# Optimization experiments

Hardware: AMD Instinct MI355X
Metric: run time of the kernel (lower is better)

Reference implementation:

```python
import jax, jax.numpy as jnp
import numpy as np

NEG_SLOPE = 0.2  # PyG GATConv default leaky_relu slope


def gat_layer(x, src, dst, W, a_src, a_dst, n_nodes, heads, ch):
    # x: [N, in_dim]; W: [in_dim, heads*ch]
    h = (x @ W).reshape(n_nodes, heads, ch)              # [N, H, C]
    e_s = jnp.einsum('nhc,hc->nh', h, a_src)             # [N, H]
    e_d = jnp.einsum('nhc,hc->nh', h, a_dst)             # [N, H]
    e = jax.nn.leaky_relu(e_s[src] + e_d[dst], NEG_SLOPE)  # [E, H]
    # segment softmax over incoming edges of each destination node
    m = jax.lax.stop_gradient(jax.ops.segment_max(e, dst, num_segments=n_nodes))
    w = jnp.exp(e - m[dst])                              # [E, H]
    z = jax.ops.segment_sum(w, dst, num_segments=n_nodes)  # [N, H]
    alpha = w / z[dst]                                   # [E, H]
    msg = h[src] * alpha[:, :, None]                     # [E, H, C]
    out = jax.ops.segment_sum(msg, dst, num_segments=n_nodes)  # [N, H, C]
    return out


def setup_inputs() -> dict:
    key = jax.random.key(0)
    ks = jax.random.split(key, 12)
    N, E, D, H = 50000, 800000, 128, 4
    x = jax.random.normal(ks[0], (N, D), dtype=jnp.float32)
    edge_index = jax.random.randint(ks[1], (2, E), 0, N, dtype=jnp.int64)
    s1 = 1.0 / np.sqrt(D)
    s2 = 1.0 / np.sqrt(D * H)
    W1 = jax.random.normal(ks[2], (D, H * D), dtype=jnp.float32) * s1
    a1_src = jax.random.normal(ks[3], (H, D), dtype=jnp.float32) * s1
    a1_dst = jax.random.normal(ks[4], (H, D), dtype=jnp.float32) * s1
    b1 = jax.random.normal(ks[5], (H * D,), dtype=jnp.float32) * 0.01
    W2 = jax.random.normal(ks[6], (H * D, D), dtype=jnp.float32) * s2
    a2_src = jax.random.normal(ks[7], (1, D), dtype=jnp.float32) * s1
    a2_dst = jax.random.normal(ks[8], (1, D), dtype=jnp.float32) * s1
    b2 = jax.random.normal(ks[9], (D,), dtype=jnp.float32) * 0.01
    fc_w = jax.random.normal(ks[10], (D, 1), dtype=jnp.float32) * s1
    fc_b = jax.random.normal(ks[11], (1,), dtype=jnp.float32) * 0.01
    return {"x": x, "edge_index": edge_index, "W1": W1, "a1_src": a1_src,
            "a1_dst": a1_dst, "b1": b1, "W2": W2, "a2_src": a2_src,
            "a2_dst": a2_dst, "b2": b2, "fc_w": fc_w, "fc_b": fc_b}


def reference(x, edge_index, W1, a1_src, a1_dst, b1, W2, a2_src, a2_dst, b2, fc_w, fc_b):
    N, D = x.shape
    H = a1_src.shape[0]
    # add self-loops (PyG GATConv default add_self_loops=True)
    loop = jnp.arange(N, dtype=edge_index.dtype)
    src = jnp.concatenate([edge_index[0], loop])
    dst = jnp.concatenate([edge_index[1], loop])
    # conv1: heads=4, concat=True -> [N, H*D]
    h1 = gat_layer(x, src, dst, W1, a1_src, a1_dst, N, H, D)
    h1 = jax.nn.relu(h1.reshape(N, H * D) + b1)
    # dropout p=0.2 is identity in eval mode
    # conv2: heads=1 -> [N, D]
    h2 = gat_layer(h1, src, dst, W2, a2_src, a2_dst, N, 1, D)
    h2 = h2.reshape(N, D) + b2
    return h2 @ fc_w + fc_b  # [N, 1]
```

## Files before the change

kernel.cpp:

```cpp
#include <hip/hip_runtime.h>
#include <cstdint>
#include <cstddef>

constexpr int kN   = 50000;
constexpr int kE   = 800000;
constexpr int kEt  = kE + kN;
constexpr float kSlope = 0.2f;
constexpr int kScanB = (kN + 255) / 256;
constexpr int kConvB = (kN * 16 + 255) / 256;
constexpr int kHistB = (kEt + 255) / 256;
constexpr int kQuarB = (kN * 16 + 255) / 256;

typedef __attribute__((ext_vector_type(8))) short bf8_t;
typedef __attribute__((ext_vector_type(4))) float f4_t;
typedef __attribute__((ext_vector_type(2))) float f2_t;

__device__ __align__(16) unsigned short g_xb[(size_t)kN * 128];
__device__ __align__(16) unsigned short g_aggx[(size_t)kN * 512];
__device__ __align__(16) unsigned short g_w1t[4 * 128 * 128];
__device__ __align__(16) float g_u[3][512];
__device__ __align__(16) float g_es1[kN * 4];
__device__ __align__(16) float g_ed1[kN * 4];
__device__ __align__(16) float2 g_sp[kN];
__device__ float g_ed2[kN];
__device__ float g_c0;
__device__ __align__(16) float g_p1s[4 * 128];
__device__ __align__(16) float g_p1d[4 * 128];
__device__ int g_deg[kN];
__device__ int g_ptr[kN + 1];
__device__ int g_rank[kEt];
__device__ int g_srcs[kEt];
__device__ int g_bsum[kScanB];

__device__ __forceinline__ float lrelu(float x) { return x > 0.f ? x : kSlope * x; }

__device__ __forceinline__ bf8_t bf8_zero() {
  uint4 z = make_uint4(0u, 0u, 0u, 0u);
  return *(bf8_t*)&z;
}

__device__ __forceinline__ unsigned short f2bf1(float v) {
  unsigned u = __float_as_uint(v);
  unsigned r = (u + 0x7FFFu + ((u >> 16) & 1u)) >> 16;
  return (unsigned short)r;
}

__global__ __launch_bounds__(256) void k_init(const float* __restrict__ x,
    const int* __restrict__ ei,
    const float* __restrict__ W1, const float* __restrict__ W2,
    const float* __restrict__ a1s, const float* __restrict__ a1d,
    const float* __restrict__ a2s, const float* __restrict__ a2d,
    const float* __restrict__ b2, const float* __restrict__ fcw,
    const float* __restrict__ fcb) {
  const int b = blockIdx.x, t = threadIdx.x;
  if (b < 197) {
    int i = b * 256 + t;
    if (i < kN) {
      g_sp[i] = make_float2(0.f, 0.f);
      g_ed2[i] = 0.f;
    }
  } else if (b < 453) {
    int gid = (b - 197) * 256 + t;
    int h = gid >> 14, rem = gid & 16383;
    int c = rem >> 7, j = rem & 127;
    float v = W1[(size_t)c * 512 + h * 128 + j];
    g_w1t[((size_t)h * 128 + j) * 128 + c] = f2bf1(v);
  } else if (b < 457) {
    int gid = (b - 453) * 256 + t;
    int which = gid >> 9, idx = gid & 511;
    int h = idx >> 7, k = idx & 127;
    const float* a = which ? a1d : a1s;
    const float* wrow = W1 + (size_t)k * 512 + h * 128;
    float s = 0.f;
#pragma unroll 8
    for (int c = 0; c < 128; ++c) s += wrow[c] * a[h * 128 + c];
    (which ? g_p1d : g_p1s)[idx] = s;
  } else if (b < 463) {
    int gid = (b - 457) * 256 + t;
    if (gid < 1536) {
      int v = gid >> 9, k = gid & 511;
      const float* vv = v == 0 ? a2s : v == 1 ? a2d : fcw;
      const float* wrow = W2 + (size_t)k * 128;
      float s = 0.f;
#pragma unroll 8
      for (int c = 0; c < 128; ++c) s += wrow[c] * vv[c];
      g_u[v][k] = s;
    }
  } else if (b < 464) {
    if (t < 64) {
      float s = b2[t] * fcw[t] + b2[64 + t] * fcw[64 + t];
#pragma unroll
      for (int off = 32; off > 0; off >>= 1) s += __shfl_down(s, off);
      if (t == 0) g_c0 = s + fcb[0];
    }
  } else if (b < 464 + kConvB) {
    int g = (b - 464) * 256 + t;
    if (g < kN * 16) {
      const float* xp = x + (size_t)g * 8;
      float4 f0 = *(const float4*)xp;
      float4 f1 = *(const float4*)(xp + 4);
      unsigned w0 = (unsigned)f2bf1(f0.x) | ((unsigned)f2bf1(f0.y) << 16);
      unsigned w1 = (unsigned)f2bf1(f0.z) | ((unsigned)f2bf1(f0.w) << 16);
      unsigned w2 = (unsigned)f2bf1(f1.x) | ((unsigned)f2bf1(f1.y) << 16);
      unsigned w3 = (unsigned)f2bf1(f1.z) | ((unsigned)f2bf1(f1.w) << 16);
      *(uint4*)(g_xb + (size_t)g * 8) = make_uint4(w0, w1, w2, w3);
    }
  } else {
    int e = (b - 464 - kConvB) * 256 + t;
    if (e < kEt) {
      int d = (e < kE) ? ei[kE + e] : e - kE;
      g_rank[e] = atomicAdd(&g_deg[d], 1);
    }
  }
}

__device__ __forceinline__ void scores1_body(const float* __restrict__ x,
                                             int bid, int t) {
  const int lane = t & 63;
  const int qt = lane >> 4, ql = lane & 15;
  const int n = ((bid * 256 + t) >> 6) * 4 + qt;
  if (n >= kN) return;
  const float* xp = x + (size_t)n * 128 + ql * 8;
  float4 xa = *(const float4*)xp;
  float4 xb = *(const float4*)(xp + 4);
  float s[4], d[4];
#pragma unroll
  for (int h = 0; h < 4; ++h) {
    const float* ps = g_p1s + h * 128 + ql * 8;
    const float* pd = g_p1d + h * 128 + ql * 8;
    s[h] = xa.x * ps[0] + xa.y * ps[1] + xa.z * ps[2] + xa.w * ps[3]
         + xb.x * ps[4] + xb.y * ps[5] + xb.z * ps[6] + xb.w * ps[7];
    d[h] = xa.x * pd[0] + xa.y * pd[1] + xa.z * pd[2] + xa.w * pd[3]
         + xb.x * pd[4] + xb.y * pd[5] + xb.z * pd[6] + xb.w * pd[7];
  }
#pragma unroll
  for (int off = 1; off < 16; off <<= 1) {
#pragma unroll
    for (int h = 0; h < 4; ++h) {
      s[h] += __shfl_xor(s[h], off);
      d[h] += __shfl_xor(d[h], off);
    }
  }
  if (ql == 0) {
    *(float4*)(g_es1 + (size_t)n * 4) = make_float4(s[0], s[1], s[2], s[3]);
    *(float4*)(g_ed1 + (size_t)n * 4) = make_float4(d[0], d[1], d[2], d[3]);
  }
}

__global__ __launch_bounds__(256) void k_scanA(const float* __restrict__ x) {
  __shared__ int s[256];
  const int b = blockIdx.x, t = threadIdx.x;
  if (b >= kScanB) {
    scores1_body(x, b - kScanB, t);
    return;
  }
  const int i = b * 256 + t;
  int d = (i < kN) ? g_deg[i] : 0;
  s[t] = d;
  __syncthreads();
  for (int off = 1; off < 256; off <<= 1) {
    int v = s[t];
    int u = (t >= off) ? s[t - off] : 0;
    __syncthreads();
    s[t] = v + u;
    __syncthreads();
  }
  if (t == 255) g_bsum[b] = s[255];
  if (i < kN) {
    g_ptr[i] = s[t] - d;
    g_deg[i] = 0;
  }
}

__global__ __launch_bounds__(256) void k_scanC() {
  __shared__ int s[256];
  const int b = blockIdx.x, t = threadIdx.x;
  int v = (t < kScanB) ? g_bsum[t] : 0;
  s[t] = v;
  __syncthreads();
  for (int off = 1; off < 256; off <<= 1) {
    int a = s[t];
    int u = (t >= off) ? s[t - off] : 0;
    __syncthreads();
    s[t] = a + u;
    __syncthreads();
  }
  const int boff = (b > 0) ? s[b - 1] : 0;
  __syncthreads();
  const int i = b * 256 + t;
  if (i < kN) g_ptr[i] = g_ptr[i] + boff;
  if (b == 0 && t == 0) g_ptr[kN] = kEt;
}

__global__ __launch_bounds__(256) void k_scatter(const int* __restrict__ ei) {
  int e = blockIdx.x * 256 + threadIdx.x;
  if (e >= kEt) return;
  int s, d;
  if (e < kE) { s = ei[e]; d = ei[kE + e]; } else { s = d = e - kE; }
  g_srcs[g_ptr[d] + g_rank[e]] = s;
}

__global__ __launch_bounds__(256) void k_agg1x() {
  const int lane = threadIdx.x & 63;
  const int qt = lane >> 4, ql = lane & 15;
  const int n = ((blockIdx.x * 256 + threadIdx.x) >> 6) * 4 + qt;
  if (n >= kN) return;
  const int beg = g_ptr[n], end = g_ptr[n + 1];
  const float4 ed = *(const float4*)(g_ed1 + (size_t)n * 4);
  const int lbase = qt * 16;
  float z0 = 0.f, z1 = 0.f, z2 = 0.f, z3 = 0.f;
  f2_t acc[4][4] = {};
  for (int base = beg; base < end; base += 16) {
    const int cnt = min(16, end - base);
    int s = 0;
    float w0 = 0.f, w1 = 0.f, w2 = 0.f, w3 = 0.f;
    if (ql < cnt) {
      s = g_srcs[base + ql];
      float4 es = *(const float4*)(g_es1 + (size_t)s * 4);
      w0 = __expf(lrelu(es.x + ed.x));
      w1 = __expf(lrelu(es.y + ed.y));
      w2 = __expf(lrelu(es.z + ed.z));
      w3 = __expf(lrelu(es.w + ed.w));
      z0 += w0; z1 += w1; z2 += w2; z3 += w3;
    }
    auto proc = [&](const uint4& uu, int e) {
      float b0 = __shfl(w0, lbase + e), b1 = __shfl(w1, lbase + e);
      float b2 = __shfl(w2, lbase + e), b3 = __shfl(w3, lbase + e);
      f2_t bb0 = b0, bb1 = b1, bb2 = b2, bb3 = b3;
      unsigned ws[4] = {uu.x, uu.y, uu.z, uu.w};
#pragma unroll
      for (int d = 0; d < 4; ++d) {
        f2_t fv;
        fv[0] = __uint_as_float(ws[d] << 16);
        fv[1] = __uint_as_float(ws[d] & 0xFFFF0000u);
        acc[0][d] += bb0 * fv;
        acc[1][d] += bb1 * fv;
        acc[2][d] += bb2 * fv;
        acc[3][d] += bb3 * fv;
      }
    };
    int e = 0;
    for (; e + 4 <= cnt; e += 4) {
      int sj0 = __shfl(s, lbase + e);
      int sj1 = __shfl(s, lbase + e + 1);
      int sj2 = __shfl(s, lbase + e + 2);
      int sj3 = __shfl(s, lbase + e + 3);
      uint4 u0 = *(const uint4*)(g_xb + (size_t)sj0 * 128 + ql * 8);
      uint4 u1 = *(const uint4*)(g_xb + (size_t)sj1 * 128 + ql * 8);
      uint4 u2 = *(const uint4*)(g_xb + (size_t)sj2 * 128 + ql * 8);
      uint4 u3 = *(const uint4*)(g_xb + (size_t)sj3 * 128 + ql * 8);
      proc(u0, e);
      proc(u1, e + 1);
      proc(u2, e + 2);
      proc(u3, e + 3);
    }
    for (; e < cnt; ++e) {
      int sj = __shfl(s, lbase + e);
      uint4 uu = *(const uint4*)(g_xb + (size_t)sj * 128 + ql * 8);
      proc(uu, e);
    }
  }
#pragma unroll
  for (int off = 1; off < 16; off <<= 1) {
    z0 += __shfl_xor(z0, off); z1 += __shfl_xor(z1, off);
    z2 += __shfl_xor(z2, off); z3 += __shfl_xor(z3, off);
  }
  const float iz[4] = {1.f / z0, 1.f / z1, 1.f / z2, 1.f / z3};
  const size_t nb = (size_t)n * 512 + ql * 8;
#pragma unroll
  for (int h = 0; h < 4; ++h) {
    unsigned wd[4];
#pragma unroll
    for (int d = 0; d < 4; ++d) {
      f2_t v = acc[h][d] * iz[h];
      wd[d] = (unsigned)f2bf1(v[0]) | ((unsigned)f2bf1(v[1]) << 16);
    }
    *(uint4*)(g_aggx + nb + h * 128) = make_uint4(wd[0], wd[1], wd[2], wd[3]);
  }
}

__global__ __launch_bounds__(256) void k_fused(const float* __restrict__ b1) {
  __shared__ float sred[2][64][3];
  const int t = threadIdx.x;
  const int lane = t & 63, w = t >> 6;
  const int wrow = w >> 1, wcol = w & 1;
  const int ln15 = lane & 15, q = lane >> 4, qo = q * 8;
  const int row0 = blockIdx.y * 64;
  const int h = blockIdx.z;

  float part[2][4][3] = {};
  f4_t h1acc[2][4] = {};
#pragma unroll
  for (int ks = 0; ks < 128; ks += 32) {
    bf8_t ah[2];
#pragma unroll
    for (int i = 0; i < 2; ++i) {
      int r = row0 + wrow * 32 + i * 16 + ln15;
      ah[i] = bf8_zero();
      if (r < kN)
        ah[i] = *(const bf8_t*)&g_aggx[(size_t)r * 512 + h * 128 + ks + qo];
    }
#pragma unroll
    for (int j = 0; j < 4; ++j) {
      size_t gb = ((size_t)h * 128 + wcol * 64 + j * 16 + ln15) * 128 + ks + qo;
      bf8_t bh = *(const bf8_t*)&g_w1t[gb];
#pragma unroll
      for (int i = 0; i < 2; ++i)
        h1acc[i][j] = __builtin_amdgcn_mfma_f32_16x16x32_bf16(ah[i], bh, h1acc[i][j], 0, 0, 0);
    }
  }
#pragma unroll
  for (int j = 0; j < 4; ++j) {
    int col = h * 128 + wcol * 64 + j * 16 + ln15;
    float bv = b1[col];
    float u0 = g_u[0][col], u1 = g_u[1][col], u2 = g_u[2][col];
#pragma unroll
    for (int i = 0; i < 2; ++i)
#pragma unroll
      for (int reg = 0; reg < 4; ++reg) {
        float v = fmaxf(h1acc[i][j][reg] + bv, 0.f);
        part[i][reg][0] += v * u0;
        part[i][reg][1] += v * u1;
        part[i][reg][2] += v * u2;
      }
  }
#pragma unroll
  for (int off = 1; off < 16; off <<= 1)
#pragma unroll
    for (int i = 0; i < 2; ++i)
#pragma unroll
      for (int reg = 0; reg < 4; ++reg)
#pragma unroll
        for (int v = 0; v < 3; ++v)
          part[i][reg][v] += __shfl_xor(part[i][reg][v], off);
  if (ln15 == 0) {
#pragma unroll
    for (int i = 0; i < 2; ++i)
#pragma unroll
      for (int reg = 0; reg < 4; ++reg) {
        int rl = wrow * 32 + i * 16 + q * 4 + reg;
#pragma unroll
        for (int v = 0; v < 3; ++v) sred[wcol][rl][v] = part[i][reg][v];
      }
  }
  __syncthreads();
  if (t < 192) {
    int row = t / 3, v = t - row * 3;
    float s = sred[0][row][v] + sred[1][row][v];
    int r = row0 + row;
    if (r < kN) {
      float* dst = v == 0 ? &g_sp[r].x : v == 1 ? &g_ed2[r] : &g_sp[r].y;
      atomicAdd(dst, s);
    }
  }
}

__global__ __launch_bounds__(256) void k_agg2s(float* __restrict__ out) {
  const int lane = threadIdx.x & 63;
  const int qt = lane >> 4, ql = lane & 15;
  const int n = ((blockIdx.x * 256 + threadIdx.x) >> 6) * 4 + qt;
  if (n >= kN) return;
  const int beg = g_ptr[n], end = g_ptr[n + 1];
  const float ed = g_ed2[n];
  float zp = 0.f, num = 0.f;
  for (int slot = beg + ql; slot < end; slot += 16) {
    int s = g_srcs[slot];
    float2 sp = g_sp[s];
    float w = __expf(lrelu(sp.x + ed));
    zp += w;
    num += w * sp.y;
  }
#pragma unroll
  for (int off = 1; off < 16; off <<= 1) {
    zp  += __shfl_xor(zp, off);
    num += __shfl_xor(num, off);
  }
  if (ql == 0) out[n] = num / zp + g_c0;
}

extern "C" void kernel_launch(void* const* d_in, const int* in_sizes, int n_in,
                              void* d_out, int out_size, void* d_ws, size_t ws_size,
                              hipStream_t stream) {
  const float* x   = (const float*)d_in[0];
  const int*   ei  = (const int*)d_in[1];
  const float* W1  = (const float*)d_in[2];
  const float* a1s = (const float*)d_in[3];
  const float* a1d = (const float*)d_in[4];
  const float* b1  = (const float*)d_in[5];
  const float* W2  = (const float*)d_in[6];
  const float* a2s = (const float*)d_in[7];
  const float* a2d = (const float*)d_in[8];
  const float* b2  = (const float*)d_in[9];
  const float* fcw = (const float*)d_in[10];
  const float* fcb = (const float*)d_in[11];
  float* out = (float*)d_out;
  (void)d_ws; (void)ws_size; (void)in_sizes; (void)n_in; (void)out_size;

  k_init<<<464 + kConvB + kHistB, 256, 0, stream>>>(x, ei, W1, W2, a1s, a1d,
                                                    a2s, a2d, b2, fcw, fcb);
  k_scanA<<<kScanB + kQuarB, 256, 0, stream>>>(x);
  k_scanC<<<kScanB, 256, 0, stream>>>();
  k_scatter<<<kHistB, 256, 0, stream>>>(ei);

  k_agg1x<<<kQuarB, 256, 0, stream>>>();

  dim3 gf(1, (kN + 63) / 64, 4);
  k_fused<<<gf, 256, 0, stream>>>(b1);

  k_agg2s<<<kQuarB, 256, 0, stream>>>(out);
}
```

Measured before the change: 267.5 us.

## Replace global atomic degree histogram with per-block LDS histograms

Destination-degree counting and per-edge rank assignment move from global atomics into 64 blocks that each build a packed 16-bit-pair histogram in shared memory over a contiguous edge chunk. A new pass reduces the per-block histograms into degrees and per-block base offsets, and scatter adds the block base to the local rank. This removes contended global atomics, but only 64 blocks run the histogram, and it adds about 12.8 MB of histogram and base traffic plus an extra kernel launch.

```diff
diff --git a/kernel.cpp b/kernel.cpp
--- a/kernel.cpp
+++ b/kernel.cpp
@@ -10,6 +10,9 @@
 constexpr int kConvB = (kN * 16 + 255) / 256;
 constexpr int kHistB = (kEt + 255) / 256;
 constexpr int kQuarB = (kN * 16 + 255) / 256;
+constexpr int kHBlk  = 64;
+constexpr int kChunk = (kEt + kHBlk - 1) / kHBlk;
+constexpr int kHalfN = kN / 2;
 
 typedef __attribute__((ext_vector_type(8))) short bf8_t;
 typedef __attribute__((ext_vector_type(4))) float f4_t;
@@ -29,6 +32,8 @@
 __device__ int g_deg[kN];
 __device__ int g_ptr[kN + 1];
 __device__ int g_rank[kEt];
+__device__ __align__(16) unsigned g_bhist[(size_t)kHBlk * kHalfN];
+__device__ __align__(16) unsigned g_bbase[(size_t)kHBlk * kHalfN];
 __device__ int g_srcs[kEt];
 __device__ int g_bsum[kScanB];
 
@@ -45,8 +50,38 @@
   return (unsigned short)r;
 }
 
+__global__ __launch_bounds__(256) void k_hist(const int* __restrict__ ei) {
+  __shared__ unsigned sh[kHalfN];
+  const int b = blockIdx.x, t = threadIdx.x;
+  for (int i = t; i < kHalfN; i += 256) sh[i] = 0u;
+  __syncthreads();
+  const int beg = b * kChunk, end = min(beg + kChunk, kEt);
+  for (int e = beg + t; e < end; e += 256) {
+    int d = (e < kE) ? ei[kE + e] : e - kE;
+    unsigned inc = (d & 1) ? 0x10000u : 1u;
+    unsigned old = atomicAdd(&sh[d >> 1], inc);
+    g_rank[e] = (d & 1) ? (int)(old >> 16) : (int)(old & 0xFFFFu);
+  }
+  __syncthreads();
+  unsigned* dst = g_bhist + (size_t)b * kHalfN;
+  for (int i = t; i < kHalfN; i += 256) dst[i] = sh[i];
+}
+
+__global__ __launch_bounds__(256) void k_pass2() {
+  const int i = blockIdx.x * 256 + threadIdx.x;
+  if (i >= kHalfN) return;
+  unsigned c0 = 0, c1 = 0;
+#pragma unroll 4
+  for (int b = 0; b < kHBlk; ++b) {
+    unsigned v = g_bhist[(size_t)b * kHalfN + i];
+    g_bbase[(size_t)b * kHalfN + i] = c0 | (c1 << 16);
+    c0 += v & 0xFFFFu;
+    c1 += v >> 16;
+  }
+  *(int2*)&g_deg[2 * i] = make_int2((int)c0, (int)c1);
+}
+
 __global__ __launch_bounds__(256) void k_init(const float* __restrict__ x,
-    const int* __restrict__ ei,
     const float* __restrict__ W1, const float* __restrict__ W2,
     const float* __restrict__ a1s, const float* __restrict__ a1d,
     const float* __restrict__ a2s, const float* __restrict__ a2d,
@@ -93,7 +128,7 @@
       for (int off = 32; off > 0; off >>= 1) s += __shfl_down(s, off);
       if (t == 0) g_c0 = s + fcb[0];
     }
-  } else if (b < 464 + kConvB) {
+  } else {
     int g = (b - 464) * 256 + t;
     if (g < kN * 16) {
       const float* xp = x + (size_t)g * 8;
@@ -105,12 +140,6 @@
       unsigned w3 = (unsigned)f2bf1(f1.z) | ((unsigned)f2bf1(f1.w) << 16);
       *(uint4*)(g_xb + (size_t)g * 8) = make_uint4(w0, w1, w2, w3);
     }
-  } else {
-    int e = (b - 464 - kConvB) * 256 + t;
-    if (e < kEt) {
-      int d = (e < kE) ? ei[kE + e] : e - kE;
-      g_rank[e] = atomicAdd(&g_deg[d], 1);
-    }
   }
 }
 
@@ -166,10 +195,7 @@
     __syncthreads();
   }
   if (t == 255) g_bsum[b] = s[255];
-  if (i < kN) {
-    g_ptr[i] = s[t] - d;
-    g_deg[i] = 0;
-  }
+  if (i < kN) g_ptr[i] = s[t] - d;
 }
 
 __global__ __launch_bounds__(256) void k_scanC() {
@@ -197,7 +223,10 @@
   if (e >= kEt) return;
   int s, d;
   if (e < kE) { s = ei[e]; d = ei[kE + e]; } else { s = d = e - kE; }
-  g_srcs[g_ptr[d] + g_rank[e]] = s;
+  const int b = e / kChunk;
+  unsigned base = g_bbase[(size_t)b * kHalfN + (d >> 1)];
+  base = (d & 1) ? (base >> 16) : (base & 0xFFFFu);
+  g_srcs[g_ptr[d] + (int)base + g_rank[e]] = s;
 }
 
 __global__ __launch_bounds__(256) void k_agg1x() {
@@ -396,8 +425,10 @@
   float* out = (float*)d_out;
   (void)d_ws; (void)ws_size; (void)in_sizes; (void)n_in; (void)out_size;
 
-  k_init<<<464 + kConvB + kHistB, 256, 0, stream>>>(x, ei, W1, W2, a1s, a1d,
-                                                    a2s, a2d, b2, fcw, fcb);
+  k_hist<<<kHBlk, 256, 0, stream>>>(ei);
+  k_init<<<464 + kConvB, 256, 0, stream>>>(x, W1, W2, a1s, a1d,
+                                           a2s, a2d, b2, fcw, fcb);
+  k_pass2<<<(kHalfN + 255) / 256, 256, 0, stream>>>();
   k_scanA<<<kScanB + kQuarB, 256, 0, stream>>>(x);
   k_scanC<<<kScanB, 256, 0, stream>>>();
   k_scatter<<<kHistB, 256, 0, stream>>>(ei);
```

After: 268.2 us. No clear change (+0.3%).
